# Optimization experiments

Hardware: AMD Instinct MI355X
Metric: run time of the kernel (lower is better)

## Reference

```python
import jax, jax.numpy as jnp
import numpy as np

HEADS = 8
DIM_HEAD = 64
EPS = 1e-6


def _layernorm(t, w, b):
    # LayerNorm over last dim (dim_head), eps=1e-6, affine
    mu = jnp.mean(t, axis=-1, keepdims=True)
    var = jnp.mean((t - mu) ** 2, axis=-1, keepdims=True)
    return (t - mu) * jax.lax.rsqrt(var + EPS) * w + b


def setup_inputs() -> dict:
    key = jax.random.key(0)
    ks = jax.random.split(key, 8)
    B, N, DIM = 2, 32768, 512
    G = 32
    inner = HEADS * DIM_HEAD
    x = jax.random.normal(ks[0], (B, N, DIM), dtype=jnp.float32)
    batch = jnp.sort(jax.random.randint(ks[1], (N,), 0, G)).astype(jnp.int32)
    w_qkv = jax.random.normal(ks[2], (3 * inner, DIM), dtype=jnp.float32) * 0.02
    ln1_w = jnp.ones((DIM_HEAD,), jnp.float32)
    ln1_b = jnp.zeros((DIM_HEAD,), jnp.float32)
    ln2_w = jnp.ones((DIM_HEAD,), jnp.float32)
    ln2_b = jnp.zeros((DIM_HEAD,), jnp.float32)
    w_out = jax.random.normal(ks[3], (DIM, inner), dtype=jnp.float32) * 0.02
    b_out = jnp.zeros((DIM,), jnp.float32)
    return {
        "x": x, "w_qkv": w_qkv,
        "ln1_w": ln1_w, "ln1_b": ln1_b, "ln2_w": ln2_w, "ln2_b": ln2_b,
        "w_out": w_out, "b_out": b_out,
        "batch": batch, "num_graphs": G,
    }


def reference(x, w_qkv, ln1_w, ln1_b, ln2_w, ln2_b, w_out, b_out, batch, num_graphs):
    B, N, DIM = x.shape
    h, d = HEADS, DIM_HEAD
    inner = h * d
    qkv = x @ w_qkv.T  # [B, N, 3*inner]
    q, k, v = jnp.split(qkv, 3, axis=-1)
    # b n (h d) -> b h n d
    to_bhnd = lambda t: t.reshape(B, N, h, d).transpose(0, 2, 1, 3)
    q, k, v = to_bhnd(q), to_bhnd(k), to_bhnd(v)
    k = _layernorm(k, ln1_w, ln1_b)
    v = _layernorm(v, ln2_w, ln2_b)

    # segment structure: one-hot [G, N] over sorted graph ids
    onehot = (batch[None, :] == jnp.arange(num_graphs)[:, None]).astype(x.dtype)
    sizes = onehot.sum(axis=1)                      # [G] graph node counts
    qn = q / sizes[batch][None, None, :, None]      # q_i / size(graph(i))

    # sequential over graphs (fixed small G); per-graph k^T v then q @ ktv,
    # accumulated in place to avoid a [G,B,h,N,d] stack.
    def body(acc, mask):
        m = mask[None, None, :, None]
        ktv = jnp.einsum('bhnd,bhne->bhde', k * m, v)     # [B,h,d,d]
        og = jnp.einsum('bhnd,bhde->bhne', qn * m, ktv)   # [B,h,N,d]
        return acc + og, None

    out, _ = jax.lax.scan(body, jnp.zeros_like(qn), onehot)
    # b h n d -> b n (h d)
    out = out.transpose(0, 2, 1, 3).reshape(B, N, inner)
    return out @ w_out.T + b_out
```

## Files before the change

### kernel.cpp

```cpp
#include <hip/hip_runtime.h>
#include <hip/hip_bf16.h>
#include <stdint.h>

#define BATCH 2
#define NN 32768
#define DIM 512
#define HEADS 8
#define INNER 512
#define G 32
#define M_ROWS (BATCH * NN)
#define MAXCHUNK 576

typedef __attribute__((ext_vector_type(8))) short bf16x8;
typedef __attribute__((ext_vector_type(4))) float floatx4;

__device__ __forceinline__ void gl_lds16(const void* g, void* l) {
    __builtin_amdgcn_global_load_lds(
        (const __attribute__((address_space(1))) uint32_t*)g,
        (__attribute__((address_space(3))) uint32_t*)l, 16, 0, 0);
}

__device__ __forceinline__ short f2bs(float f) {
    __hip_bfloat16 h = __float2bfloat16(f);
    return *reinterpret_cast<short*>(&h);
}

__device__ __forceinline__ int xcd_swizzle(int bid, int nb) {
    return (bid & 7) * (nb >> 3) + (bid >> 3);
}

__device__ __forceinline__ bf16x8 frag_ld(const char* base, int r, int quad) {
    return *reinterpret_cast<const bf16x8*>(base + r * 64 + ((quad ^ ((r >> 1) & 3)) << 4));
}

__global__ void graph_info_kernel(const int* __restrict__ batch,
                                  int* __restrict__ starts,
                                  int* __restrict__ sizes,
                                  float* __restrict__ inv,
                                  int* __restrict__ crow0,
                                  int* __restrict__ crows,
                                  int* __restrict__ cbg,
                                  int* __restrict__ cnt) {
    __shared__ int bound[G + 1];
    int g = threadIdx.x;
    if (g <= G) {
        int lo = 0, hi = NN;
        while (lo < hi) { int mid = (lo + hi) >> 1; if (batch[mid] < g) lo = mid + 1; else hi = mid; }
        bound[g] = lo;
    }
    __syncthreads();
    if (g < G) {
        int s0 = bound[g], s1 = bound[g + 1];
        starts[g] = s0;
        int c = s1 - s0;
        sizes[g] = c;
        inv[g] = c ? 1.0f / (float)c : 0.0f;
    }
    if (g == 0) {
        int c = 0;
        for (int b = 0; b < BATCH; b++)
            for (int gg = 0; gg < G; gg++) {
                int s = bound[gg], sz = bound[gg + 1] - s;
                for (int i = 0; i < sz; i += 128) {
                    crow0[c] = b * NN + s + i;
                    crows[c] = min(128, sz - i);
                    cbg[c]   = b * G + gg;
                    c++;
                }
            }
        *cnt = c;
    }
}

__global__ __launch_bounds__(256) void convert3_kernel(
        const float* __restrict__ x, const float* __restrict__ wqkv,
        const float* __restrict__ wout,
        __hip_bfloat16* __restrict__ xb, __hip_bfloat16* __restrict__ wb,
        __hip_bfloat16* __restrict__ wob) {
    int blk = blockIdx.x;
    const float* in;
    __hip_bfloat16* out;
    int i;
    if (blk < 16384)      { in = x;    out = xb;  i = blk * 256 + threadIdx.x; }
    else if (blk < 16768) { in = wqkv; out = wb;  i = (blk - 16384) * 256 + threadIdx.x; }
    else                  { in = wout; out = wob; i = (blk - 16768) * 256 + threadIdx.x; }
    const float4* p = reinterpret_cast<const float4*>(in) + (size_t)i * 2;
    float4 a = p[0], b = p[1];
    __hip_bfloat16 o[8];
    o[0] = __float2bfloat16(a.x); o[1] = __float2bfloat16(a.y);
    o[2] = __float2bfloat16(a.z); o[3] = __float2bfloat16(a.w);
    o[4] = __float2bfloat16(b.x); o[5] = __float2bfloat16(b.y);
    o[6] = __float2bfloat16(b.z); o[7] = __float2bfloat16(b.w);
    *reinterpret_cast<float4*>(out + (size_t)i * 8) = *reinterpret_cast<float4*>(o);
}

__global__ __launch_bounds__(256, 3) void qkv_gemm_kernel(
        const __hip_bfloat16* __restrict__ xb, const __hip_bfloat16* __restrict__ wb,
        const float* __restrict__ ln1w, const float* __restrict__ ln1b,
        const float* __restrict__ ln2w, const float* __restrict__ ln2b,
        const float* __restrict__ inv, const int* __restrict__ batch,
        __hip_bfloat16* __restrict__ qn, __hip_bfloat16* __restrict__ kb,
        __hip_bfloat16* __restrict__ vb) {
    __shared__ alignas(16) char smem[32768];
    int bid = xcd_swizzle(blockIdx.y * 12 + blockIdx.x, 12 * 512);
    const int row0 = (bid / 12) * 128;
    const int col0 = (bid % 12) * 128;
    const int t = threadIdx.x;
    const int lane = t & 63;
    const int wave = t >> 6;
    const int wr = wave >> 1, wc = wave & 1;
    const int quad = lane >> 4, lr = lane & 15;

    floatx4 acc[4][4] = {};

    const int srow = t >> 2;
    const int scol = (((t & 3) ^ ((t >> 3) & 3))) * 8;
    const __hip_bfloat16* gA = xb + (size_t)(row0 + srow) * DIM + scol;
    const __hip_bfloat16* gB = wb + (size_t)(col0 + srow) * DIM + scol;
    char* lA = smem + t * 16;
    char* lB = smem + 8192 + t * 16;

    gl_lds16(gA, lA);
    gl_lds16(gA + (size_t)64 * DIM, lA + 4096);
    gl_lds16(gB, lB);
    gl_lds16(gB + (size_t)64 * DIM, lB + 4096);
    __syncthreads();

    for (int it = 0; it < DIM / 32; ++it) {
        const int cb = (it & 1) << 14;
        const int nb = cb ^ 16384;
        const int k1 = (it + 1) * 32;
        if (k1 < DIM) {
            gl_lds16(gA + k1, lA + nb);
            gl_lds16(gA + (size_t)64 * DIM + k1, lA + nb + 4096);
            gl_lds16(gB + k1, lB + nb);
            gl_lds16(gB + (size_t)64 * DIM + k1, lB + nb + 4096);
        }
        bf16x8 af[4], bf[4];
        #pragma unroll
        for (int mt = 0; mt < 4; mt++)
            af[mt] = frag_ld(smem + cb, wr * 64 + mt * 16 + lr, quad);
        #pragma unroll
        for (int nt = 0; nt < 4; nt++)
            bf[nt] = frag_ld(smem + cb + 8192, wc * 64 + nt * 16 + lr, quad);
        #pragma unroll
        for (int mt = 0; mt < 4; mt++)
            #pragma unroll
            for (int nt = 0; nt < 4; nt++)
                acc[mt][nt] = __builtin_amdgcn_mfma_f32_16x16x32_bf16(af[mt], bf[nt], acc[mt][nt], 0, 0, 0);
        __syncthreads();
    }

    const int sel = (col0 + wc * 64) >> 9;
    const int hh = ((col0 + wc * 64) & 511) >> 6;

    if (sel == 0) {
        #pragma unroll
        for (int mt = 0; mt < 4; mt++) {
            #pragma unroll
            for (int reg = 0; reg < 4; reg++) {
                int row = row0 + wr * 64 + mt * 16 + quad * 4 + reg;
                int b_ = row >> 15;
                int n = row & (NN - 1);
                float s = inv[batch[n]];
                float v0 = acc[mt][0][reg] * s, v1 = acc[mt][1][reg] * s,
                      v2 = acc[mt][2][reg] * s, v3 = acc[mt][3][reg] * s;
                size_t base = ((size_t)b_ * NN + n) * INNER + hh * 64;
                qn[base + 0 * 16 + lr] = __float2bfloat16(v0);
                qn[base + 1 * 16 + lr] = __float2bfloat16(v1);
                qn[base + 2 * 16 + lr] = __float2bfloat16(v2);
                qn[base + 3 * 16 + lr] = __float2bfloat16(v3);
            }
        }
    } else {
        const float* w  = (sel == 1) ? ln1w : ln2w;
        const float* bb = (sel == 1) ? ln1b : ln2b;
        float lw[4], lb[4];
        #pragma unroll
        for (int nt = 0; nt < 4; nt++) { lw[nt] = w[nt * 16 + lr]; lb[nt] = bb[nt * 16 + lr]; }
        __hip_bfloat16* dstkv = (sel == 1) ? kb : vb;
        short* T = (short*)smem;

        #pragma unroll
        for (int mt = 0; mt < 4; mt++) {
            float f[4][4];
            #pragma unroll
            for (int reg = 0; reg < 4; reg++) {
                float v0 = acc[mt][0][reg], v1 = acc[mt][1][reg],
                      v2 = acc[mt][2][reg], v3 = acc[mt][3][reg];
                float s = v0 + v1 + v2 + v3;
                s += __shfl_xor(s, 1); s += __shfl_xor(s, 2);
                s += __shfl_xor(s, 4); s += __shfl_xor(s, 8);
                float mu = s * (1.0f / 64.0f);
                float d0 = v0 - mu, d1 = v1 - mu, d2 = v2 - mu, d3 = v3 - mu;
                float s2 = d0 * d0 + d1 * d1 + d2 * d2 + d3 * d3;
                s2 += __shfl_xor(s2, 1); s2 += __shfl_xor(s2, 2);
                s2 += __shfl_xor(s2, 4); s2 += __shfl_xor(s2, 8);
                float rstd = rsqrtf(s2 * (1.0f / 64.0f) + 1e-6f);
                f[reg][0] = d0 * rstd * lw[0] + lb[0];
                f[reg][1] = d1 * rstd * lw[1] + lb[1];
                f[reg][2] = d2 * rstd * lw[2] + lb[2];
                f[reg][3] = d3 * rstd * lw[3] + lb[3];
            }
            const int c0 = wr * 64 + mt * 16 + quad * 4;
            #pragma unroll
            for (int nt = 0; nt < 4; nt++) {
                int r = wc * 64 + nt * 16 + lr;
                int idx = r * 128 + (((c0 >> 3) ^ (r & 15)) << 3) + (c0 & 7);
                short4 pk;
                pk.x = f2bs(f[0][nt]); pk.y = f2bs(f[1][nt]);
                pk.z = f2bs(f[2][nt]); pk.w = f2bs(f[3][nt]);
                *reinterpret_cast<short4*>(&T[idx]) = pk;
            }
        }
        __syncthreads();
        const int b_ = row0 >> 15;
        const int n0 = row0 & (NN - 1);
        const int gidx = lane & 15;
        const int rbase = wave * 32 + (lane >> 4) * 8;
        short* dsts = (short*)dstkv;
        #pragma unroll
        for (int i = 0; i < 8; i++) {
            int r = rbase + i;
            int idx = r * 128 + ((gidx ^ (r & 15)) << 3);
            bf16x8 val = *reinterpret_cast<const bf16x8*>(&T[idx]);
            int j = (col0 & 511) + r;
            size_t addr = ((size_t)((b_ * HEADS + (j >> 6)) * 64 + (j & 63))) * NN
                          + n0 + gidx * 8;
            *reinterpret_cast<bf16x8*>(&dsts[addr]) = val;
        }
    }
}

__global__ __launch_bounds__(256) void ktv_w2_kernel(
        const short* __restrict__ kt, const short* __restrict__ vt,
        const short* __restrict__ wob,
        const int* __restrict__ starts, const int* __restrict__ sizes,
        short* __restrict__ w2t) {
    __shared__ alignas(16) float red[4][64][68];
    __shared__ alignas(16) short kt_sh[64][72];
    const int bhg = blockIdx.x;
    const int g = bhg & 31;
    const int bh = bhg >> 5;
    const int b = bh >> 3;
    const int h = bh & 7;
    const int s0 = starts[g];
    const int sz = sizes[g];
    const int t = threadIdx.x;
    const int lane = t & 63;
    const int w = t >> 6;
    const int quad = lane >> 4, lr = lane & 15;

    const int n0 = s0 & ~31;
    const int n1 = s0 + sz;
    const size_t base_bh = (size_t)bh * 64 * NN;

    const short* kp[4];
    const short* vp[4];
    #pragma unroll
    for (int mt = 0; mt < 4; mt++) {
        kp[mt] = kt + base_bh + (size_t)(mt * 16 + lr) * NN + quad * 8;
        vp[mt] = vt + base_bh + (size_t)(mt * 16 + lr) * NN + quad * 8;
    }

    floatx4 acc[4][4] = {};
    for (int c = n0 + w * 32; c < n1; c += 128) {
        bf16x8 af[4], bfr[4];
        if (c >= s0 && c + 32 <= n1) {
            #pragma unroll
            for (int mt = 0; mt < 4; mt++) {
                af[mt]  = *reinterpret_cast<const bf16x8*>(kp[mt] + c);
                bfr[mt] = *reinterpret_cast<const bf16x8*>(vp[mt] + c);
            }
        } else {
            #pragma unroll
            for (int mt = 0; mt < 4; mt++)
                #pragma unroll
                for (int j = 0; j < 8; j++) {
                    int n = c + quad * 8 + j;
                    bool ok = (n >= s0) && (n < n1);
                    af[mt][j]  = ok ? kp[mt][c + j] : (short)0;
                    bfr[mt][j] = ok ? vp[mt][c + j] : (short)0;
                }
        }
        #pragma unroll
        for (int mt = 0; mt < 4; mt++)
            #pragma unroll
            for (int et = 0; et < 4; et++)
                acc[mt][et] = __builtin_amdgcn_mfma_f32_16x16x32_bf16(af[mt], bfr[et], acc[mt][et], 0, 0, 0);
    }

    #pragma unroll
    for (int mt = 0; mt < 4; mt++)
        #pragma unroll
        for (int et = 0; et < 4; et++)
            *reinterpret_cast<floatx4*>(&red[w][lane][(mt * 4 + et) * 4]) = acc[mt][et];
    __syncthreads();
    {
        const int mt = w;
        #pragma unroll
        for (int et = 0; et < 4; et++) {
            floatx4 s = *reinterpret_cast<const floatx4*>(&red[0][lane][(mt * 4 + et) * 4]);
            #pragma unroll
            for (int w2 = 1; w2 < 4; w2++)
                s += *reinterpret_cast<const floatx4*>(&red[w2][lane][(mt * 4 + et) * 4]);
            #pragma unroll
            for (int reg = 0; reg < 4; reg++)
                kt_sh[mt * 16 + quad * 4 + reg][et * 16 + lr] = f2bs(s[reg]);
        }
    }
    __syncthreads();

    const short* wsl = wob + h * 64;
    short* w2 = w2t + (size_t)(b * G + g) * 512 * 512 + h * 64;
    bf16x8 b0[4], b1[4];
    #pragma unroll
    for (int dt = 0; dt < 4; dt++) {
        b0[dt] = *reinterpret_cast<const bf16x8*>(&kt_sh[dt * 16 + lr][quad * 8]);
        b1[dt] = *reinterpret_cast<const bf16x8*>(&kt_sh[dt * 16 + lr][quad * 8 + 32]);
    }
    for (int ct = 0; ct < 8; ct++) {
        int c = w * 128 + ct * 16 + lr;
        bf16x8 a0 = *reinterpret_cast<const bf16x8*>(wsl + (size_t)c * INNER + quad * 8);
        bf16x8 a1 = *reinterpret_cast<const bf16x8*>(wsl + (size_t)c * INNER + 32 + quad * 8);
        #pragma unroll
        for (int dt = 0; dt < 4; dt++) {
            floatx4 d = {0.f, 0.f, 0.f, 0.f};
            d = __builtin_amdgcn_mfma_f32_16x16x32_bf16(a0, b0[dt], d, 0, 0, 0);
            d = __builtin_amdgcn_mfma_f32_16x16x32_bf16(a1, b1[dt], d, 0, 0, 0);
            #pragma unroll
            for (int reg = 0; reg < 4; reg++) {
                int crow = w * 128 + ct * 16 + quad * 4 + reg;
                w2[(size_t)crow * 512 + dt * 16 + lr] = f2bs(d[reg]);
            }
        }
    }
}

__global__ __launch_bounds__(256, 3) void final_gemm_kernel(
        const __hip_bfloat16* __restrict__ qn, const __hip_bfloat16* __restrict__ w2t,
        const float* __restrict__ bias,
        const int* __restrict__ crow0, const int* __restrict__ crows,
        const int* __restrict__ cbg, const int* __restrict__ cnt,
        float* __restrict__ out) {
    __shared__ alignas(16) char smem[32768];
    int bid = xcd_swizzle(blockIdx.y * 4 + blockIdx.x, 4 * MAXCHUNK);
    const int chunk = bid >> 2;
    if (chunk >= *cnt) return;
    const int row0  = crow0[chunk];
    const int nrows = crows[chunk];
    const int bg    = cbg[chunk];
    const int col0 = (bid & 3) * 128;
    const int t = threadIdx.x;
    const int lane = t & 63;
    const int wave = t >> 6;
    const int wr = wave >> 1, wc = wave & 1;
    const int quad = lane >> 4, lr = lane & 15;

    floatx4 acc[4][4] = {};

    const int srow = t >> 2;
    const int scol = (((t & 3) ^ ((t >> 3) & 3))) * 8;
    const __hip_bfloat16* gA = qn + (size_t)(row0 + srow) * INNER + scol;
    const __hip_bfloat16* gB = w2t + (size_t)bg * 512 * 512 + (size_t)(col0 + srow) * 512 + scol;
    char* lA = smem + t * 16;
    char* lB = smem + 8192 + t * 16;

    gl_lds16(gA, lA);
    gl_lds16(gA + (size_t)64 * INNER, lA + 4096);
    gl_lds16(gB, lB);
    gl_lds16(gB + (size_t)64 * 512, lB + 4096);
    __syncthreads();

    for (int it = 0; it < INNER / 32; ++it) {
        const int cb = (it & 1) << 14;
        const int nb = cb ^ 16384;
        const int k1 = (it + 1) * 32;
        if (k1 < INNER) {
            gl_lds16(gA + k1, lA + nb);
            gl_lds16(gA + (size_t)64 * INNER + k1, lA + nb + 4096);
            gl_lds16(gB + k1, lB + nb);
            gl_lds16(gB + (size_t)64 * 512 + k1, lB + nb + 4096);
        }
        bf16x8 af[4], bf[4];
        #pragma unroll
        for (int mt = 0; mt < 4; mt++)
            af[mt] = frag_ld(smem + cb, wr * 64 + mt * 16 + lr, quad);
        #pragma unroll
        for (int nt = 0; nt < 4; nt++)
            bf[nt] = frag_ld(smem + cb + 8192, wc * 64 + nt * 16 + lr, quad);
        #pragma unroll
        for (int mt = 0; mt < 4; mt++)
            #pragma unroll
            for (int nt = 0; nt < 4; nt++)
                acc[mt][nt] = __builtin_amdgcn_mfma_f32_16x16x32_bf16(af[mt], bf[nt], acc[mt][nt], 0, 0, 0);
        __syncthreads();
    }

    #pragma unroll
    for (int nt = 0; nt < 4; nt++) {
        int col = col0 + wc * 64 + nt * 16 + lr;
        float bv = bias[col];
        #pragma unroll
        for (int mt = 0; mt < 4; mt++)
            #pragma unroll
            for (int reg = 0; reg < 4; reg++) {
                int rl = wr * 64 + mt * 16 + quad * 4 + reg;
                if (rl < nrows)
                    out[(size_t)(row0 + rl) * DIM + col] = acc[mt][nt][reg] + bv;
            }
    }
}

extern "C" void kernel_launch(void* const* d_in, const int* in_sizes, int n_in,
                              void* d_out, int out_size, void* d_ws, size_t ws_size,
                              hipStream_t stream) {
    const float* x     = (const float*)d_in[0];
    const float* w_qkv = (const float*)d_in[1];
    const float* ln1w  = (const float*)d_in[2];
    const float* ln1b  = (const float*)d_in[3];
    const float* ln2w  = (const float*)d_in[4];
    const float* ln2b  = (const float*)d_in[5];
    const float* w_out = (const float*)d_in[6];
    const float* b_out = (const float*)d_in[7];
    const int*   batch = (const int*)d_in[8];
    float* out = (float*)d_out;

    char* ws = (char*)d_ws;
    const size_t MB = 1u << 20;
    __hip_bfloat16* qn  = (__hip_bfloat16*)(ws);
    __hip_bfloat16* kb  = (__hip_bfloat16*)(ws + 64 * MB);
    __hip_bfloat16* vb  = (__hip_bfloat16*)(ws + 128 * MB);
    __hip_bfloat16* xb  = (__hip_bfloat16*)(ws + 192 * MB);
    __hip_bfloat16* w2t = (__hip_bfloat16*)(ws + 192 * MB);
    __hip_bfloat16* wb  = (__hip_bfloat16*)(ws + 256 * MB);
    __hip_bfloat16* wob = (__hip_bfloat16*)(ws + 258 * MB);
    char* meta = ws + 259 * MB;
    int*   starts = (int*)(meta);
    int*   sizes  = (int*)(meta + 128);
    float* inv    = (float*)(meta + 256);
    int*   crow0  = (int*)(meta + 512);
    int*   crows  = (int*)(meta + 512 + 4096);
    int*   cbg    = (int*)(meta + 512 + 8192);
    int*   cnt    = (int*)(meta + 512 + 12288);

    graph_info_kernel<<<1, 64, 0, stream>>>(batch, starts, sizes, inv,
                                            crow0, crows, cbg, cnt);
    convert3_kernel<<<16896, 256, 0, stream>>>(x, w_qkv, w_out, xb, wb, wob);
    qkv_gemm_kernel<<<dim3((3 * INNER) / 128, M_ROWS / 128), 256, 0, stream>>>(
        xb, wb, ln1w, ln1b, ln2w, ln2b, inv, batch, qn, kb, vb);
    ktv_w2_kernel<<<BATCH * HEADS * G, 256, 0, stream>>>(
        (const short*)kb, (const short*)vb, (const short*)wob, starts, sizes, (short*)w2t);
    final_gemm_kernel<<<dim3(4, MAXCHUNK), 256, 0, stream>>>(
        qn, w2t, b_out, crow0, crows, cbg, cnt, out);
}
```

Measured before the change: 556.6 us.

## Enlarge QKV GEMM tile to 256x256 with 8 waves and deeper LDS pipeline

Rewrites the QKV projection GEMM to use 256x256 output tiles with 512 threads, 128KB of dynamic LDS, and a double-buffered K=64 stage that interleaves global-to-LDS loads with MFMA phases, using explicit barriers and s_setprio. The larger tile raises arithmetic intensity and reuse of the A and B tiles. The epilogue for the LayerNorm'd K/V transpose is reworked for the new tile shape. The cost is higher register pressure (8x4 accumulators per wave), lower occupancy, and fragile manual waitcnt and barrier logic.

```diff
diff --git a/kernel.cpp b/kernel.cpp
--- a/kernel.cpp
+++ b/kernel.cpp
@@ -10,6 +10,7 @@
 #define G 32
 #define M_ROWS (BATCH * NN)
 #define MAXCHUNK 576
+#define NKT 8
 
 typedef __attribute__((ext_vector_type(8))) short bf16x8;
 typedef __attribute__((ext_vector_type(4))) float floatx4;
@@ -94,100 +95,122 @@
     *reinterpret_cast<float4*>(out + (size_t)i * 8) = *reinterpret_cast<float4*>(o);
 }
 
-__global__ __launch_bounds__(256, 3) void qkv_gemm_kernel(
+__global__ __launch_bounds__(512, 2) void qkv_gemm_kernel(
         const __hip_bfloat16* __restrict__ xb, const __hip_bfloat16* __restrict__ wb,
         const float* __restrict__ ln1w, const float* __restrict__ ln1b,
         const float* __restrict__ ln2w, const float* __restrict__ ln2b,
         const float* __restrict__ inv, const int* __restrict__ batch,
         __hip_bfloat16* __restrict__ qn, __hip_bfloat16* __restrict__ kb,
         __hip_bfloat16* __restrict__ vb) {
-    __shared__ alignas(16) char smem[32768];
-    int bid = xcd_swizzle(blockIdx.y * 12 + blockIdx.x, 12 * 512);
-    const int row0 = (bid / 12) * 128;
-    const int col0 = (bid % 12) * 128;
+    extern __shared__ char smem[];
+    int bid = xcd_swizzle(blockIdx.y * 6 + blockIdx.x, 6 * 256);
+    const int row0 = (bid / 6) * 256;
+    const int col0 = (bid % 6) * 256;
     const int t = threadIdx.x;
     const int lane = t & 63;
     const int wave = t >> 6;
-    const int wr = wave >> 1, wc = wave & 1;
+    const int wr = wave >> 2;
+    const int wc = wave & 3;
     const int quad = lane >> 4, lr = lane & 15;
 
-    floatx4 acc[4][4] = {};
+    floatx4 acc[8][4] = {};
 
     const int srow = t >> 2;
     const int scol = (((t & 3) ^ ((t >> 3) & 3))) * 8;
     const __hip_bfloat16* gA = xb + (size_t)(row0 + srow) * DIM + scol;
     const __hip_bfloat16* gB = wb + (size_t)(col0 + srow) * DIM + scol;
-    char* lA = smem + t * 16;
-    char* lB = smem + 8192 + t * 16;
-
-    gl_lds16(gA, lA);
-    gl_lds16(gA + (size_t)64 * DIM, lA + 4096);
-    gl_lds16(gB, lB);
-    gl_lds16(gB + (size_t)64 * DIM, lB + 4096);
-    __syncthreads();
-
-    for (int it = 0; it < DIM / 32; ++it) {
-        const int cb = (it & 1) << 14;
-        const int nb = cb ^ 16384;
-        const int k1 = (it + 1) * 32;
-        if (k1 < DIM) {
-            gl_lds16(gA + k1, lA + nb);
-            gl_lds16(gA + (size_t)64 * DIM + k1, lA + nb + 4096);
-            gl_lds16(gB + k1, lB + nb);
-            gl_lds16(gB + (size_t)64 * DIM + k1, lB + nb + 4096);
-        }
-        bf16x8 af[4], bf[4];
-        #pragma unroll
-        for (int mt = 0; mt < 4; mt++)
-            af[mt] = frag_ld(smem + cb, wr * 64 + mt * 16 + lr, quad);
-        #pragma unroll
-        for (int nt = 0; nt < 4; nt++)
-            bf[nt] = frag_ld(smem + cb + 8192, wc * 64 + nt * 16 + lr, quad);
-        #pragma unroll
-        for (int mt = 0; mt < 4; mt++)
-            #pragma unroll
-            for (int nt = 0; nt < 4; nt++)
-                acc[mt][nt] = __builtin_amdgcn_mfma_f32_16x16x32_bf16(af[mt], bf[nt], acc[mt][nt], 0, 0, 0);
-        __syncthreads();
-    }
-
-    const int sel = (col0 + wc * 64) >> 9;
-    const int hh = ((col0 + wc * 64) & 511) >> 6;
+
+    #pragma unroll
+    for (int r = 0; r < 4; ++r) {
+        const int isB = r & 1, ks = r >> 1;
+        char* dst = smem + isB * 65536 + ks * 16384 + t * 16;
+        const __hip_bfloat16* src = (isB ? gB : gA) + ks * 32;
+        gl_lds16(src, dst);
+        gl_lds16(src + (size_t)128 * DIM, dst + 8192);
+    }
+    asm volatile("s_waitcnt vmcnt(4)" ::: "memory");
+    __builtin_amdgcn_s_barrier();
+
+    for (int kt = 0; kt < NKT; ++kt) {
+        const int cb = (kt & 1) << 15;
+        const int nb = ((kt + 1) & 1) << 15;
+        bf16x8 bfr[4];
+        #pragma unroll
+        for (int p = 0; p < 4; ++p) {
+            const int ks = p >> 1;
+            if ((p & 1) == 0) {
+                #pragma unroll
+                for (int n = 0; n < 4; ++n)
+                    bfr[n] = frag_ld(smem + 65536 + cb + ks * 16384,
+                                     wc * 64 + n * 16 + lr, quad);
+            }
+            bf16x8 afr[4];
+            #pragma unroll
+            for (int i = 0; i < 4; ++i)
+                afr[i] = frag_ld(smem + cb + ks * 16384,
+                                 wr * 128 + ((p & 1) * 4 + i) * 16 + lr, quad);
+            if (kt + 1 < NKT) {
+                const int isB = p & 1, ks2 = p >> 1;
+                char* dst = smem + isB * 65536 + nb + ks2 * 16384 + t * 16;
+                const __hip_bfloat16* src = (isB ? gB : gA) + (kt + 1) * 64 + ks2 * 32;
+                gl_lds16(src, dst);
+                gl_lds16(src + (size_t)128 * DIM, dst + 8192);
+            }
+            __builtin_amdgcn_s_barrier();
+            asm volatile("s_waitcnt lgkmcnt(0)" ::: "memory");
+            __builtin_amdgcn_sched_barrier(0);
+            __builtin_amdgcn_s_setprio(1);
+            #pragma unroll
+            for (int i = 0; i < 4; ++i)
+                #pragma unroll
+                for (int n = 0; n < 4; ++n)
+                    acc[(p & 1) * 4 + i][n] = __builtin_amdgcn_mfma_f32_16x16x32_bf16(
+                        afr[i], bfr[n], acc[(p & 1) * 4 + i][n], 0, 0, 0);
+            __builtin_amdgcn_s_setprio(0);
+            if (p & 1) {
+                if (kt < NKT - 1)
+                    asm volatile("s_waitcnt vmcnt(4)" ::: "memory");
+                else
+                    asm volatile("s_waitcnt vmcnt(0)" ::: "memory");
+            }
+            __builtin_amdgcn_s_barrier();
+        }
+    }
+
+    const int colw = col0 + wc * 64;
+    const int sel = colw >> 9;
+    const int hh  = (colw & 511) >> 6;
+    const int b_  = row0 >> 15;
+    const int n0  = row0 & (NN - 1);
 
     if (sel == 0) {
         #pragma unroll
-        for (int mt = 0; mt < 4; mt++) {
-            #pragma unroll
-            for (int reg = 0; reg < 4; reg++) {
-                int row = row0 + wr * 64 + mt * 16 + quad * 4 + reg;
-                int b_ = row >> 15;
-                int n = row & (NN - 1);
+        for (int m = 0; m < 8; ++m) {
+            #pragma unroll
+            for (int reg = 0; reg < 4; ++reg) {
+                int n = n0 + wr * 128 + m * 16 + quad * 4 + reg;
                 float s = inv[batch[n]];
-                float v0 = acc[mt][0][reg] * s, v1 = acc[mt][1][reg] * s,
-                      v2 = acc[mt][2][reg] * s, v3 = acc[mt][3][reg] * s;
                 size_t base = ((size_t)b_ * NN + n) * INNER + hh * 64;
-                qn[base + 0 * 16 + lr] = __float2bfloat16(v0);
-                qn[base + 1 * 16 + lr] = __float2bfloat16(v1);
-                qn[base + 2 * 16 + lr] = __float2bfloat16(v2);
-                qn[base + 3 * 16 + lr] = __float2bfloat16(v3);
+                #pragma unroll
+                for (int nf = 0; nf < 4; ++nf)
+                    qn[base + nf * 16 + lr] = __float2bfloat16(acc[m][nf][reg] * s);
             }
         }
     } else {
         const float* w  = (sel == 1) ? ln1w : ln2w;
         const float* bb = (sel == 1) ? ln1b : ln2b;
-        float lw[4], lb[4];
-        #pragma unroll
-        for (int nt = 0; nt < 4; nt++) { lw[nt] = w[nt * 16 + lr]; lb[nt] = bb[nt * 16 + lr]; }
-        __hip_bfloat16* dstkv = (sel == 1) ? kb : vb;
+        float lw[4], lb2[4];
+        #pragma unroll
+        for (int nf = 0; nf < 4; ++nf) { lw[nf] = w[nf * 16 + lr]; lb2[nf] = bb[nf * 16 + lr]; }
         short* T = (short*)smem;
 
         #pragma unroll
-        for (int mt = 0; mt < 4; mt++) {
+        for (int m = 0; m < 8; ++m) {
             float f[4][4];
             #pragma unroll
-            for (int reg = 0; reg < 4; reg++) {
-                float v0 = acc[mt][0][reg], v1 = acc[mt][1][reg],
-                      v2 = acc[mt][2][reg], v3 = acc[mt][3][reg];
+            for (int reg = 0; reg < 4; ++reg) {
+                float v0 = acc[m][0][reg], v1 = acc[m][1][reg],
+                      v2 = acc[m][2][reg], v3 = acc[m][3][reg];
                 float s = v0 + v1 + v2 + v3;
                 s += __shfl_xor(s, 1); s += __shfl_xor(s, 2);
                 s += __shfl_xor(s, 4); s += __shfl_xor(s, 8);
@@ -197,37 +220,34 @@
                 s2 += __shfl_xor(s2, 1); s2 += __shfl_xor(s2, 2);
                 s2 += __shfl_xor(s2, 4); s2 += __shfl_xor(s2, 8);
                 float rstd = rsqrtf(s2 * (1.0f / 64.0f) + 1e-6f);
-                f[reg][0] = d0 * rstd * lw[0] + lb[0];
-                f[reg][1] = d1 * rstd * lw[1] + lb[1];
-                f[reg][2] = d2 * rstd * lw[2] + lb[2];
-                f[reg][3] = d3 * rstd * lw[3] + lb[3];
-            }
-            const int c0 = wr * 64 + mt * 16 + quad * 4;
-            #pragma unroll
-            for (int nt = 0; nt < 4; nt++) {
-                int r = wc * 64 + nt * 16 + lr;
-                int idx = r * 128 + (((c0 >> 3) ^ (r & 15)) << 3) + (c0 & 7);
+                f[reg][0] = d0 * rstd * lw[0] + lb2[0];
+                f[reg][1] = d1 * rstd * lw[1] + lb2[1];
+                f[reg][2] = d2 * rstd * lw[2] + lb2[2];
+                f[reg][3] = d3 * rstd * lw[3] + lb2[3];
+            }
+            const int nloc0 = wr * 128 + m * 16 + quad * 4;
+            const int glw = nloc0 >> 3, hw = (nloc0 >> 2) & 1;
+            #pragma unroll
+            for (int nf = 0; nf < 4; ++nf) {
+                int dloc = wc * 64 + nf * 16 + lr;
+                int gs = glw ^ (dloc & 7);
                 short4 pk;
-                pk.x = f2bs(f[0][nt]); pk.y = f2bs(f[1][nt]);
-                pk.z = f2bs(f[2][nt]); pk.w = f2bs(f[3][nt]);
-                *reinterpret_cast<short4*>(&T[idx]) = pk;
+                pk.x = f2bs(f[0][nf]); pk.y = f2bs(f[1][nf]);
+                pk.z = f2bs(f[2][nf]); pk.w = f2bs(f[3][nf]);
+                *reinterpret_cast<short4*>((char*)T + dloc * 512 + gs * 16 + hw * 8) = pk;
             }
         }
         __syncthreads();
-        const int b_ = row0 >> 15;
-        const int n0 = row0 & (NN - 1);
-        const int gidx = lane & 15;
-        const int rbase = wave * 32 + (lane >> 4) * 8;
-        short* dsts = (short*)dstkv;
-        #pragma unroll
-        for (int i = 0; i < 8; i++) {
-            int r = rbase + i;
-            int idx = r * 128 + ((gidx ^ (r & 15)) << 3);
-            bf16x8 val = *reinterpret_cast<const bf16x8*>(&T[idx]);
-            int j = (col0 & 511) + r;
-            size_t addr = ((size_t)((b_ * HEADS + (j >> 6)) * 64 + (j & 63))) * NN
-                          + n0 + gidx * 8;
-            *reinterpret_cast<bf16x8*>(&dsts[addr]) = val;
+        const int dloc = t >> 1;
+        const int j = (col0 & 511) + dloc;
+        short* dsts = (short*)((sel == 1) ? kb : vb);
+        size_t rowbase = ((size_t)((b_ * HEADS + (j >> 6)) * 64 + (j & 63))) * NN + n0;
+        #pragma unroll
+        for (int i = 0; i < 16; ++i) {
+            int gl = (t & 1) * 16 + i;
+            int gs = gl ^ (dloc & 7);
+            bf16x8 val = *reinterpret_cast<const bf16x8*>((char*)T + dloc * 512 + gs * 16);
+            *reinterpret_cast<bf16x8*>(&dsts[rowbase + gl * 8]) = val;
         }
     }
 }
@@ -343,7 +363,7 @@
         const int* __restrict__ crow0, const int* __restrict__ crows,
         const int* __restrict__ cbg, const int* __restrict__ cnt,
         float* __restrict__ out) {
-    __shared__ alignas(16) char smem[32768];
+    __shared__ alignas(16) char smem2[32768];
     int bid = xcd_swizzle(blockIdx.y * 4 + blockIdx.x, 4 * MAXCHUNK);
     const int chunk = bid >> 2;
     if (chunk >= *cnt) return;
@@ -363,8 +383,8 @@
     const int scol = (((t & 3) ^ ((t >> 3) & 3))) * 8;
     const __hip_bfloat16* gA = qn + (size_t)(row0 + srow) * INNER + scol;
     const __hip_bfloat16* gB = w2t + (size_t)bg * 512 * 512 + (size_t)(col0 + srow) * 512 + scol;
-    char* lA = smem + t * 16;
-    char* lB = smem + 8192 + t * 16;
+    char* lA = smem2 + t * 16;
+    char* lB = smem2 + 8192 + t * 16;
 
     gl_lds16(gA, lA);
     gl_lds16(gA + (size_t)64 * INNER, lA + 4096);
@@ -385,10 +405,10 @@
         bf16x8 af[4], bf[4];
         #pragma unroll
         for (int mt = 0; mt < 4; mt++)
-            af[mt] = frag_ld(smem + cb, wr * 64 + mt * 16 + lr, quad);
+            af[mt] = frag_ld(smem2 + cb, wr * 64 + mt * 16 + lr, quad);
         #pragma unroll
         for (int nt = 0; nt < 4; nt++)
-            bf[nt] = frag_ld(smem + cb + 8192, wc * 64 + nt * 16 + lr, quad);
+            bf[nt] = frag_ld(smem2 + cb + 8192, wc * 64 + nt * 16 + lr, quad);
         #pragma unroll
         for (int mt = 0; mt < 4; mt++)
             #pragma unroll
@@ -444,10 +464,17 @@
     int*   cbg    = (int*)(meta + 512 + 8192);
     int*   cnt    = (int*)(meta + 512 + 12288);
 
+    static bool attr_set = false;
+    if (!attr_set) {
+        hipFuncSetAttribute(reinterpret_cast<const void*>(qkv_gemm_kernel),
+                            hipFuncAttributeMaxDynamicSharedMemorySize, 131072);
+        attr_set = true;
+    }
+
     graph_info_kernel<<<1, 64, 0, stream>>>(batch, starts, sizes, inv,
                                             crow0, crows, cbg, cnt);
     convert3_kernel<<<16896, 256, 0, stream>>>(x, w_qkv, w_out, xb, wb, wob);
-    qkv_gemm_kernel<<<dim3((3 * INNER) / 128, M_ROWS / 128), 256, 0, stream>>>(
+    qkv_gemm_kernel<<<dim3(6, M_ROWS / 256), 512, 131072, stream>>>(
         xb, wb, ln1w, ln1b, ln2w, ln2b, inv, batch, qn, kb, vb);
     ktv_w2_kernel<<<BATCH * HEADS * G, 256, 0, stream>>>(
         (const short*)kb, (const short*)vb, (const short*)wob, starts, sizes, (short*)w2t);
```

New measurement: 574.9 us. 3.3% more time.
